# Performance work log

Hardware: AMD Instinct MI355X
Metric: run time of the kernel (lower is better)

Reference implementation:

```python
import jax, jax.numpy as jnp
import numpy as np

N_NODES = 50000
N_EDGES = 800000
IN_CH = 64
HID = 128
LAST_HID = 256


def setup_inputs() -> dict:
    key = jax.random.key(0)
    ks = jax.random.split(key, 12)
    x = jax.random.normal(ks[0], (N_NODES, IN_CH), dtype=jnp.float32)
    edge_index = jax.random.randint(ks[1], (2, N_EDGES), 0, N_NODES, dtype=jnp.int64)
    s = lambda fan_in: 1.0 / np.sqrt(fan_in)
    return {
        "x": x,
        "edge_index": edge_index,
        # SAGEConv1: lin_l (aggregated neighbors, with bias), lin_r (root, no bias)
        "W1l": jax.random.normal(ks[2], (HID, IN_CH), dtype=jnp.float32) * s(IN_CH),
        "b1l": jnp.zeros((HID,), dtype=jnp.float32),
        "W1r": jax.random.normal(ks[3], (HID, IN_CH), dtype=jnp.float32) * s(IN_CH),
        # SAGEConv2 -> 1 channel
        "W2l": jax.random.normal(ks[4], (1, HID), dtype=jnp.float32) * s(HID),
        "b2l": jnp.zeros((1,), dtype=jnp.float32),
        "W2r": jax.random.normal(ks[5], (1, HID), dtype=jnp.float32) * s(HID),
        # fc1 (LazyLinear bound to N_NODES input features) and fc2
        "fc1_W": jax.random.normal(ks[6], (LAST_HID, N_NODES), dtype=jnp.float32) * s(N_NODES),
        "fc1_b": jnp.zeros((LAST_HID,), dtype=jnp.float32),
        "fc2_W": jax.random.normal(ks[7], (1, LAST_HID), dtype=jnp.float32) * s(LAST_HID),
        "fc2_b": jnp.zeros((1,), dtype=jnp.float32),
    }


def _sage_conv(h, src, dst, Wl, bl, Wr, n_nodes):
    # PyG SAGEConv (mean aggr): out = lin_l(mean_{j in N(i)} x_j) + lin_r(x_i)
    msgs = h[src]  # [E, F] gather of source node features
    summed = jax.ops.segment_sum(msgs, dst, num_segments=n_nodes)  # [N, F]
    deg = jax.ops.segment_sum(jnp.ones((src.shape[0],), h.dtype), dst, num_segments=n_nodes)
    agg = summed / jnp.maximum(deg, 1.0)[:, None]
    return agg @ Wl.T + bl + h @ Wr.T


def reference(x, edge_index, W1l, b1l, W1r, W2l, b2l, W2r, fc1_W, fc1_b, fc2_W, fc2_b):
    n = x.shape[0]
    src, dst = edge_index[0], edge_index[1]
    h = jax.nn.relu(_sage_conv(x, src, dst, W1l, b1l, W1r, n))   # [N, HID]
    h = jax.nn.relu(_sage_conv(h, src, dst, W2l, b2l, W2r, n))   # [N, 1]
    v = h[:, 0]                                                   # [N]
    z = fc1_W @ v + fc1_b                                         # [LAST_HID]
    pred = fc2_W @ z + fc2_b                                      # [1]
    return pred[0]  # scalar (torch.squeeze)
```

## Files before the change

kernel.cpp:

```cpp
#include <hip/hip_runtime.h>

#define N_NODESC 50000
#define N_EDGESC 800000
#define MAXDEG 64

typedef short bf16x8 __attribute__((ext_vector_type(8)));
typedef short short4v __attribute__((ext_vector_type(4)));
typedef unsigned short ushort4v __attribute__((ext_vector_type(4)));
typedef float f32x4  __attribute__((ext_vector_type(4)));

__device__ inline unsigned short f2bf(float f) {
    unsigned u = __float_as_uint(f);
    unsigned r = u + 0x7FFFu + ((u >> 16) & 1u);
    return (unsigned short)(r >> 16);
}
__device__ inline float bf2f(unsigned short h) {
    return __uint_as_float(((unsigned)h) << 16);
}

__global__ void kW0_init_pack(const float* __restrict__ x,
                              const float* __restrict__ W1l, const float* __restrict__ W1r,
                              short* __restrict__ pkhi, short* __restrict__ pklo,
                              unsigned short* __restrict__ xb,
                              int* __restrict__ deg, float* __restrict__ z) {
    int i = blockIdx.x * 256 + threadIdx.x;
    if (i < N_NODESC) deg[i] = 0;
    if (i < 256) z[i] = 0.0f;

    int base = i * 16;
    if (base < N_NODESC * 64) {
        const float* src = x + base;
        bf16x8 h0, h1;
        #pragma unroll
        for (int j = 0; j < 2; j++) {
            float4 a = *(const float4*)(src + j * 8);
            float4 b = *(const float4*)(src + j * 8 + 4);
            bf16x8& hh = j ? h1 : h0;
            hh[0] = (short)f2bf(a.x); hh[1] = (short)f2bf(a.y);
            hh[2] = (short)f2bf(a.z); hh[3] = (short)f2bf(a.w);
            hh[4] = (short)f2bf(b.x); hh[5] = (short)f2bf(b.y);
            hh[6] = (short)f2bf(b.z); hh[7] = (short)f2bf(b.w);
        }
        *(bf16x8*)(xb + base) = h0;
        *(bf16x8*)(xb + base + 8) = h1;
    }

    if (blockIdx.x < 4) {
        int ks = blockIdx.x;
        int t  = threadIdx.x;
        int o  = t & 127;
        int h  = t >> 7;
        const float* src = (ks < 2) ? (W1r + o * 64 + ks * 32)
                                    : (W1l + o * 64 + (ks - 2) * 32);
        #pragma unroll
        for (int qi = 0; qi < 2; qi++) {
            int q = 2 * h + qi;
            float4 a = *(const float4*)(src + q * 8);
            float4 b = *(const float4*)(src + q * 8 + 4);
            float v[8] = {a.x, a.y, a.z, a.w, b.x, b.y, b.z, b.w};
            bf16x8 hv, lv;
            #pragma unroll
            for (int j = 0; j < 8; j++) {
                unsigned short hh = f2bf(v[j]);
                hv[j] = (short)hh;
                lv[j] = (short)f2bf(v[j] - bf2f(hh));
            }
            int idx = ((ks * 4 + q) * 128 + o) * 8;
            *(bf16x8*)&pkhi[idx] = hv;
            *(bf16x8*)&pklo[idx] = lv;
        }
    }
}

#define K1_BLOCKS 2048
#define K1_EPB (N_EDGESC / (K1_BLOCKS / 8))
__global__ void k1_bucket(const int* __restrict__ ei, int* __restrict__ deg,
                          unsigned short* __restrict__ bucket) {
    int g   = blockIdx.x & 7;
    int idx = blockIdx.x >> 3;
    int lo = g * (N_NODESC / 8), hi = lo + (N_NODESC / 8);
    int e0 = idx * K1_EPB;
    for (int i = threadIdx.x; i < K1_EPB; i += 256) {
        int e = e0 + i;
        int dst = ei[N_EDGESC + e];
        if (dst >= lo && dst < hi) {
            int src = ei[e];
            int slot = atomicAdd(&deg[dst], 1);
            if (slot < MAXDEG) bucket[dst * MAXDEG + slot] = (unsigned short)src;
        }
    }
}

#define K3S 144
#define K3BLK 32

__launch_bounds__(512, 4)
__global__ void k3_fused(const float* __restrict__ x, const unsigned short* __restrict__ xb,
                         const int* __restrict__ deg, const unsigned short* __restrict__ bucket,
                         const short* __restrict__ pkhi, const short* __restrict__ pklo,
                         const float* __restrict__ b1l,
                         const float* __restrict__ W2l, const float* __restrict__ W2r,
                         float* __restrict__ s_out, float* __restrict__ t_out) {
    __shared__ __align__(16) short sAhi[K3BLK * K3S];
    __shared__ __align__(16) short sAlo[K3BLK * K3S];
    __shared__ __align__(16) unsigned short sBkt[K3BLK * 64];
    __shared__ int sDeg[K3BLK];
    __shared__ float sSp[8][K3BLK], sTp[8][K3BLK];

    int tid = threadIdx.x;
    int lane = tid & 63;
    int wave = tid >> 6;
    int col = lane & 15;
    int quad = lane >> 4;
    int node0 = blockIdx.x * K3BLK;

    float4 sv;
    {
        int n = tid >> 4, kc = tid & 15;
        int node = node0 + n;
        if (node < N_NODESC) {
            sv = *(const float4*)(x + node * 64 + kc * 4);
        } else {
            sv = make_float4(0.f, 0.f, 0.f, 0.f);
        }
    }

    {
        int off = tid * 4;
        int glim = (N_NODESC - node0) * 64;
        if (off + 4 <= glim) {
            *(ushort4v*)&sBkt[off] = *(const ushort4v*)&bucket[node0 * 64 + off];
        } else {
            #pragma unroll
            for (int k = 0; k < 4; k++)
                sBkt[off + k] = (off + k < glim) ? bucket[node0 * 64 + off + k]
                                                 : (unsigned short)0;
        }
        if (tid < K3BLK) {
            int node = node0 + tid;
            sDeg[tid] = (node < N_NODESC) ? deg[node] : 0;
        }
    }

    {
        int n = tid >> 4, kc = tid & 15;
        float v[4] = {sv.x, sv.y, sv.z, sv.w};
        short4v hv, lv;
        #pragma unroll
        for (int j = 0; j < 4; j++) {
            unsigned short h = f2bf(v[j]);
            hv[j] = (short)h;
            lv[j] = (short)f2bf(v[j] - bf2f(h));
        }
        *(short4v*)&sAhi[n * K3S + kc * 4] = hv;
        *(short4v*)&sAlo[n * K3S + kc * 4] = lv;
    }
    __syncthreads();

    #pragma unroll
    for (int c4 = 0; c4 < 4; c4++) {
        int nloc = wave * 4 + c4;
        int d = sDeg[nloc];
        int c = min(d, MAXDEG);
        float a0 = 0.f, a1 = 0.f, a2 = 0.f, a3 = 0.f;
        float a4 = 0.f, a5 = 0.f, a6 = 0.f, a7 = 0.f;
        int j = 0;
        for (; j + 8 <= c; j += 8) {
            ushort4v q0 = *(const ushort4v*)&sBkt[nloc * 64 + j];
            ushort4v q1 = *(const ushort4v*)&sBkt[nloc * 64 + j + 4];
            a0 += bf2f(xb[(int)q0[0] * 64 + lane]);
            a1 += bf2f(xb[(int)q0[1] * 64 + lane]);
            a2 += bf2f(xb[(int)q0[2] * 64 + lane]);
            a3 += bf2f(xb[(int)q0[3] * 64 + lane]);
            a4 += bf2f(xb[(int)q1[0] * 64 + lane]);
            a5 += bf2f(xb[(int)q1[1] * 64 + lane]);
            a6 += bf2f(xb[(int)q1[2] * 64 + lane]);
            a7 += bf2f(xb[(int)q1[3] * 64 + lane]);
        }
        for (; j < c; j++) {
            a0 += bf2f(xb[(int)sBkt[nloc * 64 + j] * 64 + lane]);
        }
        float av = ((a0 + a1) + (a2 + a3)) + ((a4 + a5) + (a6 + a7));
        float inv = 1.0f / (float)max(d, 1);
        float m = av * inv;
        unsigned short h = f2bf(m);
        unsigned short l = f2bf(m - bf2f(h));
        sAhi[nloc * K3S + 64 + lane] = (short)h;
        sAlo[nloc * K3S + 64 + lane] = (short)l;
    }

    int o = wave * 16 + col;
    bf16x8 bhi[4], blo[4];
    float bias_r = b1l[o], w2l_r = W2l[o], w2r_r = W2r[o];
    #pragma unroll
    for (int ks = 0; ks < 4; ks++) {
        int idx = ((ks * 4 + quad) * 128 + o) * 8;
        bhi[ks] = *(const bf16x8*)&pkhi[idx];
        blo[ks] = *(const bf16x8*)&pklo[idx];
    }
    __syncthreads();

    f32x4 acc[2];
    acc[0] = (f32x4)0.f;
    acc[1] = (f32x4)0.f;

    #pragma unroll
    for (int ks = 0; ks < 4; ks++) {
        #pragma unroll
        for (int nt = 0; nt < 2; nt++) {
            int off = (nt * 16 + col) * K3S + ks * 32 + quad * 8;
            bf16x8 ah = *(const bf16x8*)&sAhi[off];
            bf16x8 al = *(const bf16x8*)&sAlo[off];
            acc[nt] = __builtin_amdgcn_mfma_f32_16x16x32_bf16(ah, bhi[ks], acc[nt], 0, 0, 0);
            acc[nt] = __builtin_amdgcn_mfma_f32_16x16x32_bf16(al, bhi[ks], acc[nt], 0, 0, 0);
            acc[nt] = __builtin_amdgcn_mfma_f32_16x16x32_bf16(ah, blo[ks], acc[nt], 0, 0, 0);
        }
    }

    #pragma unroll
    for (int nt = 0; nt < 2; nt++) {
        float sp[4], tp[4];
        #pragma unroll
        for (int reg = 0; reg < 4; reg++) {
            float h = fmaxf(acc[nt][reg] + bias_r, 0.f);
            sp[reg] = h * w2l_r;
            tp[reg] = h * w2r_r;
        }
        #pragma unroll
        for (int reg = 0; reg < 4; reg++) {
            #pragma unroll
            for (int m = 1; m <= 8; m <<= 1) {
                sp[reg] += __shfl_xor(sp[reg], m);
                tp[reg] += __shfl_xor(tp[reg], m);
            }
        }
        if (col == 0) {
            int nn = nt * 16 + quad * 4;
            #pragma unroll
            for (int reg = 0; reg < 4; reg++) {
                sSp[wave][nn + reg] = sp[reg];
                sTp[wave][nn + reg] = tp[reg];
            }
        }
    }
    __syncthreads();
    if (tid < K3BLK) {
        int node = node0 + tid;
        if (node < N_NODESC) {
            float ssum = 0.f, tsum = 0.f;
            #pragma unroll
            for (int w = 0; w < 8; w++) { ssum += sSp[w][tid]; tsum += sTp[w][tid]; }
            s_out[node] = ssum;
            t_out[node] = tsum;
        }
    }
}

__global__ void k4_layer2(const float* __restrict__ s, const float* __restrict__ t,
                          const int* __restrict__ deg, const unsigned short* __restrict__ bucket,
                          const float* __restrict__ b2l, float* __restrict__ v) {
    int tid = threadIdx.x;
    int lane = tid & 15;
    int node = blockIdx.x * 16 + (tid >> 4);
    int d = deg[node];
    int c = min(d, MAXDEG);
    float sum = 0.f;
    for (int k = lane; k < c; k += 16) sum += s[bucket[node * MAXDEG + k]];
    sum += __shfl_xor(sum, 1);
    sum += __shfl_xor(sum, 2);
    sum += __shfl_xor(sum, 4);
    sum += __shfl_xor(sum, 8);
    if (lane == 0) {
        float h = sum / (float)max(d, 1) + b2l[0] + t[node];
        v[node] = fmaxf(h, 0.f);
    }
}

__global__ void k5_fc1(const float* __restrict__ fc1W, const float* __restrict__ v,
                       float* __restrict__ z) {
    int row = blockIdx.x >> 2;
    int part = blockIdx.x & 3;
    const float4* W4 = (const float4*)(fc1W + row * 50000 + part * 12500);
    const float4* v4 = (const float4*)(v + part * 12500);
    float sum = 0.f;
    for (int i = threadIdx.x; i < 3125; i += 256) {
        float4 w = W4[i], a = v4[i];
        sum += w.x * a.x + w.y * a.y + w.z * a.z + w.w * a.w;
    }
    #pragma unroll
    for (int m = 1; m < 64; m <<= 1) sum += __shfl_xor(sum, m);
    __shared__ float red[4];
    if ((threadIdx.x & 63) == 0) red[threadIdx.x >> 6] = sum;
    __syncthreads();
    if (threadIdx.x == 0) atomicAdd(&z[row], red[0] + red[1] + red[2] + red[3]);
}

__global__ void k6_head(const float* __restrict__ z, const float* __restrict__ fc1b,
                        const float* __restrict__ fc2W, const float* __restrict__ fc2b,
                        float* __restrict__ out) {
    int t = threadIdx.x;
    float val = (z[t] + fc1b[t]) * fc2W[t];
    #pragma unroll
    for (int m = 1; m < 64; m <<= 1) val += __shfl_xor(val, m);
    __shared__ float red[4];
    if ((t & 63) == 0) red[t >> 6] = val;
    __syncthreads();
    if (t == 0) out[0] = red[0] + red[1] + red[2] + red[3] + fc2b[0];
}

extern "C" void kernel_launch(void* const* d_in, const int* in_sizes, int n_in,
                              void* d_out, int out_size, void* d_ws, size_t ws_size,
                              hipStream_t stream) {
    const float* x    = (const float*)d_in[0];
    const int*   ei   = (const int*)d_in[1];
    const float* W1l  = (const float*)d_in[2];
    const float* b1l  = (const float*)d_in[3];
    const float* W1r  = (const float*)d_in[4];
    const float* W2l  = (const float*)d_in[5];
    const float* b2l  = (const float*)d_in[6];
    const float* W2r  = (const float*)d_in[7];
    const float* fc1W = (const float*)d_in[8];
    const float* fc1b = (const float*)d_in[9];
    const float* fc2W = (const float*)d_in[10];
    const float* fc2b = (const float*)d_in[11];
    float* out = (float*)d_out;

    char* ws = (char*)d_ws;
    int*            deg    = (int*)           (ws + 0);
    float*          z      = (float*)         (ws + 200192);
    unsigned short* bucket = (unsigned short*)(ws + 201216);
    unsigned short* xb     = (unsigned short*)(ws + 6601216);
    float*          s      = (float*)         (ws + 13001216);
    float*          t      = (float*)         (ws + 13201216);
    float*          v      = (float*)         (ws + 13401216);
    short*          pkhi   = (short*)         (ws + 13601280);
    short*          pklo   = (short*)         (ws + 13634048);

    kW0_init_pack<<<782,  256, 0, stream>>>(x, W1l, W1r, pkhi, pklo, xb, deg, z);
    k1_bucket    <<<K1_BLOCKS, 256, 0, stream>>>(ei, deg, bucket);
    k3_fused     <<<1563, 512, 0, stream>>>(x, xb, deg, bucket, pkhi, pklo, b1l, W2l, W2r, s, t);
    k4_layer2    <<<3125, 256, 0, stream>>>(s, t, deg, bucket, b2l, v);
    k5_fc1       <<<1024, 256, 0, stream>>>(fc1W, v, z);
    k6_head      <<<1,    256, 0, stream>>>(z, fc1b, fc2W, fc2b, out);
}
```

Measured before the change: 203.8 us.

## Bucket edges with LDS degree counters and split neighbor gather into own kernel

Edge bucketing changes from a global-atomic scheme over 8 destination ranges to 64 blocks of 1024 threads. Each block owns a node range, scans all destination indices, and counts degrees with LDS atomics before writing them back. The neighbor-mean gather moves out of the fused GEMM kernel into a separate high-occupancy kernel that writes fp32 aggregates, and the GEMM kernel now just loads x and agg. This trades an extra 12.8MB write/read round trip and a kernel launch for better latency hiding in the gather, while the 64-block bucket kernel reads every edge index 64 times.

```diff
diff --git a/kernel.cpp b/kernel.cpp
--- a/kernel.cpp
+++ b/kernel.cpp
@@ -22,9 +22,8 @@
                               const float* __restrict__ W1l, const float* __restrict__ W1r,
                               short* __restrict__ pkhi, short* __restrict__ pklo,
                               unsigned short* __restrict__ xb,
-                              int* __restrict__ deg, float* __restrict__ z) {
+                              float* __restrict__ z) {
     int i = blockIdx.x * 256 + threadIdx.x;
-    if (i < N_NODESC) deg[i] = 0;
     if (i < 256) z[i] = 0.0f;
 
     int base = i * 16;
@@ -72,39 +71,80 @@
     }
 }
 
-#define K1_BLOCKS 2048
-#define K1_EPB (N_EDGESC / (K1_BLOCKS / 8))
+#define K1_NB 64
+#define K1_NPB 782
+__launch_bounds__(1024)
 __global__ void k1_bucket(const int* __restrict__ ei, int* __restrict__ deg,
                           unsigned short* __restrict__ bucket) {
-    int g   = blockIdx.x & 7;
-    int idx = blockIdx.x >> 3;
-    int lo = g * (N_NODESC / 8), hi = lo + (N_NODESC / 8);
-    int e0 = idx * K1_EPB;
-    for (int i = threadIdx.x; i < K1_EPB; i += 256) {
-        int e = e0 + i;
-        int dst = ei[N_EDGESC + e];
-        if (dst >= lo && dst < hi) {
-            int src = ei[e];
-            int slot = atomicAdd(&deg[dst], 1);
-            if (slot < MAXDEG) bucket[dst * MAXDEG + slot] = (unsigned short)src;
-        }
-    }
+    __shared__ int sdeg[K1_NPB];
+    int tid = threadIdx.x;
+    int lo = blockIdx.x * K1_NPB;
+    int hi = min(lo + K1_NPB, N_NODESC);
+    int cnt = hi - lo;
+    for (int i = tid; i < cnt; i += 1024) sdeg[i] = 0;
+    __syncthreads();
+
+    const int4* dst4 = (const int4*)(ei + N_EDGESC);
+    for (int e4 = tid; e4 < N_EDGESC / 4; e4 += 1024) {
+        int4 d4 = dst4[e4];
+        int dv[4] = {d4.x, d4.y, d4.z, d4.w};
+        #pragma unroll
+        for (int k = 0; k < 4; k++) {
+            int dst = dv[k];
+            if (dst >= lo && dst < hi) {
+                int src = ei[e4 * 4 + k];
+                int slot = atomicAdd(&sdeg[dst - lo], 1);
+                if (slot < MAXDEG) bucket[dst * MAXDEG + slot] = (unsigned short)src;
+            }
+        }
+    }
+    __syncthreads();
+    for (int i = tid; i < cnt; i += 1024) deg[lo + i] = sdeg[i];
+}
+
+__global__ void k2_gather(const unsigned short* __restrict__ xb,
+                          const int* __restrict__ deg,
+                          const unsigned short* __restrict__ bucket,
+                          float* __restrict__ agg) {
+    __shared__ unsigned short sB[4][64];
+    int tid = threadIdx.x;
+    int wave = tid >> 6, lane = tid & 63;
+    int node = blockIdx.x * 4 + wave;
+    sB[wave][lane] = bucket[node * MAXDEG + lane];
+    int d = deg[node];
+    int c = min(d, MAXDEG);
+    float a0 = 0.f, a1 = 0.f, a2 = 0.f, a3 = 0.f;
+    float a4 = 0.f, a5 = 0.f, a6 = 0.f, a7 = 0.f;
+    int j = 0;
+    for (; j + 8 <= c; j += 8) {
+        a0 += bf2f(xb[(int)sB[wave][j + 0] * 64 + lane]);
+        a1 += bf2f(xb[(int)sB[wave][j + 1] * 64 + lane]);
+        a2 += bf2f(xb[(int)sB[wave][j + 2] * 64 + lane]);
+        a3 += bf2f(xb[(int)sB[wave][j + 3] * 64 + lane]);
+        a4 += bf2f(xb[(int)sB[wave][j + 4] * 64 + lane]);
+        a5 += bf2f(xb[(int)sB[wave][j + 5] * 64 + lane]);
+        a6 += bf2f(xb[(int)sB[wave][j + 6] * 64 + lane]);
+        a7 += bf2f(xb[(int)sB[wave][j + 7] * 64 + lane]);
+    }
+    for (; j < c; j++) {
+        a0 += bf2f(xb[(int)sB[wave][j] * 64 + lane]);
+    }
+    float av = ((a0 + a1) + (a2 + a3)) + ((a4 + a5) + (a6 + a7));
+    float inv = 1.0f / (float)max(d, 1);
+    agg[node * 64 + lane] = av * inv;
 }
 
 #define K3S 144
 #define K3BLK 32
 
 __launch_bounds__(512, 4)
-__global__ void k3_fused(const float* __restrict__ x, const unsigned short* __restrict__ xb,
-                         const int* __restrict__ deg, const unsigned short* __restrict__ bucket,
-                         const short* __restrict__ pkhi, const short* __restrict__ pklo,
-                         const float* __restrict__ b1l,
-                         const float* __restrict__ W2l, const float* __restrict__ W2r,
-                         float* __restrict__ s_out, float* __restrict__ t_out) {
+__global__ void k3_mm(const float* __restrict__ x, const float* __restrict__ agg,
+                      const short* __restrict__ pkhi, const short* __restrict__ pklo,
+                      const float* __restrict__ b1l,
+                      const float* __restrict__ W2l, const float* __restrict__ W2r,
+                      float* __restrict__ s_out, float* __restrict__ t_out) {
     __shared__ __align__(16) short sAhi[K3BLK * K3S];
     __shared__ __align__(16) short sAlo[K3BLK * K3S];
-    __shared__ __align__(16) unsigned short sBkt[K3BLK * 64];
-    __shared__ int sDeg[K3BLK];
     __shared__ float sSp[8][K3BLK], sTp[8][K3BLK];
 
     int tid = threadIdx.x;
@@ -114,37 +154,25 @@
     int quad = lane >> 4;
     int node0 = blockIdx.x * K3BLK;
 
-    float4 sv;
-    {
-        int n = tid >> 4, kc = tid & 15;
+    float4 sv[2];
+    #pragma unroll
+    for (int i = 0; i < 2; i++) {
+        int c = tid + 512 * i;
+        int n = c >> 5, kc = c & 31;
         int node = node0 + n;
         if (node < N_NODESC) {
-            sv = *(const float4*)(x + node * 64 + kc * 4);
+            const float* src = (kc < 16) ? (x + node * 64 + kc * 4)
+                                         : (agg + node * 64 + (kc - 16) * 4);
+            sv[i] = *(const float4*)src;
         } else {
-            sv = make_float4(0.f, 0.f, 0.f, 0.f);
-        }
-    }
-
-    {
-        int off = tid * 4;
-        int glim = (N_NODESC - node0) * 64;
-        if (off + 4 <= glim) {
-            *(ushort4v*)&sBkt[off] = *(const ushort4v*)&bucket[node0 * 64 + off];
-        } else {
-            #pragma unroll
-            for (int k = 0; k < 4; k++)
-                sBkt[off + k] = (off + k < glim) ? bucket[node0 * 64 + off + k]
-                                                 : (unsigned short)0;
-        }
-        if (tid < K3BLK) {
-            int node = node0 + tid;
-            sDeg[tid] = (node < N_NODESC) ? deg[node] : 0;
-        }
-    }
-
-    {
-        int n = tid >> 4, kc = tid & 15;
-        float v[4] = {sv.x, sv.y, sv.z, sv.w};
+            sv[i] = make_float4(0.f, 0.f, 0.f, 0.f);
+        }
+    }
+    #pragma unroll
+    for (int i = 0; i < 2; i++) {
+        int c = tid + 512 * i;
+        int n = c >> 5, kc = c & 31;
+        float v[4] = {sv[i].x, sv[i].y, sv[i].z, sv[i].w};
         short4v hv, lv;
         #pragma unroll
         for (int j = 0; j < 4; j++) {
@@ -154,39 +182,6 @@
         }
         *(short4v*)&sAhi[n * K3S + kc * 4] = hv;
         *(short4v*)&sAlo[n * K3S + kc * 4] = lv;
-    }
-    __syncthreads();
-
-    #pragma unroll
-    for (int c4 = 0; c4 < 4; c4++) {
-        int nloc = wave * 4 + c4;
-        int d = sDeg[nloc];
-        int c = min(d, MAXDEG);
-        float a0 = 0.f, a1 = 0.f, a2 = 0.f, a3 = 0.f;
-        float a4 = 0.f, a5 = 0.f, a6 = 0.f, a7 = 0.f;
-        int j = 0;
-        for (; j + 8 <= c; j += 8) {
-            ushort4v q0 = *(const ushort4v*)&sBkt[nloc * 64 + j];
-            ushort4v q1 = *(const ushort4v*)&sBkt[nloc * 64 + j + 4];
-            a0 += bf2f(xb[(int)q0[0] * 64 + lane]);
-            a1 += bf2f(xb[(int)q0[1] * 64 + lane]);
-            a2 += bf2f(xb[(int)q0[2] * 64 + lane]);
-            a3 += bf2f(xb[(int)q0[3] * 64 + lane]);
-            a4 += bf2f(xb[(int)q1[0] * 64 + lane]);
-            a5 += bf2f(xb[(int)q1[1] * 64 + lane]);
-            a6 += bf2f(xb[(int)q1[2] * 64 + lane]);
-            a7 += bf2f(xb[(int)q1[3] * 64 + lane]);
-        }
-        for (; j < c; j++) {
-            a0 += bf2f(xb[(int)sBkt[nloc * 64 + j] * 64 + lane]);
-        }
-        float av = ((a0 + a1) + (a2 + a3)) + ((a4 + a5) + (a6 + a7));
-        float inv = 1.0f / (float)max(d, 1);
-        float m = av * inv;
-        unsigned short h = f2bf(m);
-        unsigned short l = f2bf(m - bf2f(h));
-        sAhi[nloc * K3S + 64 + lane] = (short)h;
-        sAlo[nloc * K3S + 64 + lane] = (short)l;
     }
 
     int o = wave * 16 + col;
@@ -330,16 +325,18 @@
     float*          z      = (float*)         (ws + 200192);
     unsigned short* bucket = (unsigned short*)(ws + 201216);
     unsigned short* xb     = (unsigned short*)(ws + 6601216);
-    float*          s      = (float*)         (ws + 13001216);
-    float*          t      = (float*)         (ws + 13201216);
-    float*          v      = (float*)         (ws + 13401216);
-    short*          pkhi   = (short*)         (ws + 13601280);
-    short*          pklo   = (short*)         (ws + 13634048);
-
-    kW0_init_pack<<<782,  256, 0, stream>>>(x, W1l, W1r, pkhi, pklo, xb, deg, z);
-    k1_bucket    <<<K1_BLOCKS, 256, 0, stream>>>(ei, deg, bucket);
-    k3_fused     <<<1563, 512, 0, stream>>>(x, xb, deg, bucket, pkhi, pklo, b1l, W2l, W2r, s, t);
-    k4_layer2    <<<3125, 256, 0, stream>>>(s, t, deg, bucket, b2l, v);
-    k5_fc1       <<<1024, 256, 0, stream>>>(fc1W, v, z);
-    k6_head      <<<1,    256, 0, stream>>>(z, fc1b, fc2W, fc2b, out);
-}
+    float*          agg    = (float*)         (ws + 13001216);
+    float*          s      = (float*)         (ws + 25801216);
+    float*          t      = (float*)         (ws + 26001216);
+    float*          v      = (float*)         (ws + 26201216);
+    short*          pkhi   = (short*)         (ws + 26401280);
+    short*          pklo   = (short*)         (ws + 26434048);
+
+    kW0_init_pack<<<782,   256, 0, stream>>>(x, W1l, W1r, pkhi, pklo, xb, z);
+    k1_bucket    <<<K1_NB, 1024, 0, stream>>>(ei, deg, bucket);
+    k2_gather    <<<12500, 256, 0, stream>>>(xb, deg, bucket, agg);
+    k3_mm        <<<1563,  512, 0, stream>>>(x, agg, pkhi, pklo, b1l, W2l, W2r, s, t);
+    k4_layer2    <<<3125,  256, 0, stream>>>(s, t, deg, bucket, b2l, v);
+    k5_fc1       <<<1024,  256, 0, stream>>>(fc1W, v, z);
+    k6_head      <<<1,     256, 0, stream>>>(z, fc1b, fc2W, fc2b, out);
+}
```

After: 401.4 us. 1.97x slower.
